# Performance work log

Hardware: AMD Instinct MI355X
Metric: run time of the kernel (lower is better)

Reference implementation:

```python
import jax, jax.numpy as jnp
import numpy as np

B, T, C = 2, 1024, 256
DH = 8          # deformable head num
HD = 64         # head_dim
HN = C // HD    # head_num = 4


def grid_sample_bilinear(img, grid):
    """torch.nn.functional.grid_sample (bilinear, align_corners=True) for a
    single-channel image. img: (B,H,W); grid: (B,Ho,Wo,2) with grid[...,0]=x
    (width coord), grid[...,1]=y (height coord), both in [-1,1]."""
    B_, H, W = img.shape
    gx = (grid[..., 0] + 1.0) * 0.5 * (W - 1)
    gy = (grid[..., 1] + 1.0) * 0.5 * (H - 1)
    x0 = jnp.floor(gx)
    y0 = jnp.floor(gy)
    wx = gx - x0
    wy = gy - y0
    flat_img = img.reshape(B_, -1)

    def gather(iy, ix):
        iy = jnp.clip(iy.astype(jnp.int32), 0, H - 1)
        ix = jnp.clip(ix.astype(jnp.int32), 0, W - 1)
        flat = (iy * W + ix).reshape(B_, -1)
        return jnp.take_along_axis(flat_img, flat, axis=1).reshape(iy.shape)

    out = (gather(y0, x0) * (1 - wy) * (1 - wx)
           + gather(y0, x0 + 1) * (1 - wy) * wx
           + gather(y0 + 1, x0) * wy * (1 - wx)
           + gather(y0 + 1, x0 + 1) * wy * wx)
    return out  # (B, Ho, Wo)


def setup_inputs() -> dict:
    key = jax.random.key(0)
    ks = jax.random.split(key, 8)
    s = 1.0 / np.sqrt(C)
    return {
        "x": jax.random.normal(ks[0], (B, T, C), jnp.float32),
        "W_off1": jax.random.normal(ks[1], (C, C), jnp.float32) * s,
        "b_off1": jnp.zeros((C,), jnp.float32),
        "W_off2": jax.random.normal(ks[2], (C, DH * C * 2), jnp.float32) * s,
        "b_off2": jnp.zeros((DH * C * 2,), jnp.float32),
        "Wq": jax.random.normal(ks[3], (C, C), jnp.float32) * s,
        "bq": jnp.zeros((C,), jnp.float32),
        "Wk": jax.random.normal(ks[4], (C, C), jnp.float32) * s,
        "bk": jnp.zeros((C,), jnp.float32),
        "Wv": jax.random.normal(ks[5], (C, C), jnp.float32) * s,
        "bv": jnp.zeros((C,), jnp.float32),
        "Wo": jax.random.normal(ks[6], (DH * C, C), jnp.float32) / np.sqrt(DH * C),
        "bo": jnp.zeros((C,), jnp.float32),
    }


def reference(x, W_off1, b_off1, W_off2, b_off2, Wq, bq, Wk, bk, Wv, bv, Wo, bo):
    B_, T_, C_ = x.shape
    # offset network: per-token MLP -> DH heads of (C,2) grid coords in [-1,1]
    h = jax.nn.gelu(x @ W_off1 + b_off1)
    off = jnp.tanh((h @ W_off2 + b_off2).reshape(B_, T_, DH, C_, 2))
    off = off.transpose(0, 2, 1, 3, 4).reshape(B_, DH * T_, C_, 2)
    # deformable token resampling: x tiled DH times along token axis acts as
    # a 1-channel image of size (DH*T, C); grid_sample(bilinear, align_corners)
    img = jnp.tile(x, (1, DH, 1))                       # B x (DH*T) x C
    xs = grid_sample_bilinear(img, off)                 # B x (DH*T) x C
    xs = xs.reshape(B_ * DH, T_, C_)
    # multi-head attention over resampled tokens
    q = (xs @ Wq + bq).reshape(B_ * DH, T_, HN, HD)
    k = (xs @ Wk + bk).reshape(B_ * DH, T_, HN, HD)
    v = (xs @ Wv + bv).reshape(B_ * DH, T_, HN, HD)
    scores = jnp.einsum('bnhd,bkhd->bhnk', q, k) / np.float32(np.sqrt(HD))
    A = jax.nn.softmax(scores, axis=-1)
    out = jnp.einsum('bhnk,bkhd->bnhd', A, v).reshape(B_ * DH, T_, HN * HD)
    # gather deformable heads back and project
    out = out.reshape(B_, DH, T_, HN * HD).transpose(0, 2, 1, 3).reshape(B_, T_, DH * HN * HD)
    return out @ Wo + bo
```

## Files before the change

### kernel.cpp

```cpp
#include <hip/hip_runtime.h>
#include <hip/hip_bf16.h>

typedef __attribute__((ext_vector_type(8))) _Float16 half8;
typedef __attribute__((ext_vector_type(4))) _Float16 half4;
typedef __attribute__((ext_vector_type(4))) float f32x4;
typedef __attribute__((ext_vector_type(16))) float f32x16;
typedef __attribute__((ext_vector_type(2))) unsigned uint2v;
typedef __attribute__((ext_vector_type(4))) unsigned uint4v;

#define MFMAH(a, b, c) __builtin_amdgcn_mfma_f32_16x16x32_f16((a), (b), (c), 0, 0, 0)
#define MFMA32(a, b, c) __builtin_amdgcn_mfma_f32_32x32x16_f16((a), (b), (c), 0, 0, 0)

__device__ __forceinline__ short f2h(float v) { _Float16 h = (_Float16)v; return __builtin_bit_cast(short, h); }
__device__ __forceinline__ f32x4 fzero() { f32x4 z = {0.f, 0.f, 0.f, 0.f}; return z; }
__device__ __forceinline__ float u2f(unsigned u) { return __builtin_bit_cast(float, u); }
__device__ __forceinline__ unsigned f2u(float f) { return __builtin_bit_cast(unsigned, f); }

__device__ __forceinline__ void gl16(const void* g, void* l) {
    __builtin_amdgcn_global_load_lds((const __attribute__((address_space(1))) unsigned*)g,
                                     (__attribute__((address_space(3))) unsigned*)l, 16, 0, 0);
}

__device__ __forceinline__ float fast_tanh(float z) {
    float E = __expf(2.f * z);
    return 1.f - 2.f / (E + 1.f);
}

__device__ __forceinline__ float gelu_tanh(float v) {
    float u = 0.7978845608028654f * (v + 0.044715f * v * v * v);
    return 0.5f * v * (1.f + fast_tanh(u));
}


__global__ __launch_bounds__(256) void prep_all_k(
    const float* __restrict__ x, const float* __restrict__ Woff2,
    const float* __restrict__ Wq, const float* __restrict__ Wk, const float* __restrict__ Wv,
    const float* __restrict__ Wo,
    short* __restrict__ B2T, short* __restrict__ Wtqkv, short* __restrict__ WtoT,
    half4* __restrict__ Q)
{
    __shared__ float t[64][65];
    const int tid = threadIdx.x;
    const int bid = blockIdx.x;
    if (bid < 256) {
        const int bk = bid >> 6, bn = bid & 63;
        const int k0 = bk * 64, n0 = bn * 64;
#pragma unroll
        for (int p = 0; p < 16; ++p) {
            int idx = p * 256 + tid, r = idx >> 6, c = idx & 63;
            t[r][c] = Woff2[(long)(k0 + r) * 4096 + n0 + c];
        }
        __syncthreads();
#pragma unroll
        for (int p = 0; p < 16; ++p) {
            int idx = p * 256 + tid, nr = idx >> 6, kc = idx & 63;
            float v = t[kc][nr];
            _Float16 w1 = (_Float16)v;
            _Float16 w2 = (_Float16)(v - (float)w1);
            long base = (long)(n0 + nr) * 768 + k0 + kc;
            B2T[base]       = __builtin_bit_cast(short, w1);
            B2T[base + 256] = __builtin_bit_cast(short, w1);
            B2T[base + 512] = __builtin_bit_cast(short, w2);
        }
    } else if (bid < 1024) {
        int i = (bid - 256) * 256 + tid;
        int n = i >> 8, k = i & 255;
        const float* s = (n < 256) ? Wq : (n < 512) ? Wk : Wv;
        Wtqkv[i] = f2h(s[k * 256 + (n & 255)]);
    } else if (bid < 3072) {
        int i = (bid - 1024) * 256 + tid;
        int n = i >> 11, k = i & 2047;
        WtoT[i] = f2h(Wo[k * 256 + n]);
    } else {
        int i = (bid - 3072) * 256 + tid;
        int b = i >> 18, r = (i >> 8) & 1023, c = i & 255;
        const float* xb = x + (b << 18);
        int r1 = (r + 1) & 1023, c1 = (c + 1) & 255;
        half4 qv;
        qv[0] = (_Float16)xb[(r << 8) + c];
        qv[1] = (_Float16)xb[(r << 8) + c1];
        qv[2] = (_Float16)xb[(r1 << 8) + c];
        qv[3] = (_Float16)xb[(r1 << 8) + c1];
        Q[i] = qv;
    }
}


__global__ __launch_bounds__(256) void gemm1_k(const float* __restrict__ x, const float* __restrict__ W,
                                               const float* __restrict__ bias, short* __restrict__ hs) {
    __shared__ float As[64][17];
    __shared__ float Bs[16][68];
    const int tid = threadIdx.x;
    const int bm = blockIdx.x >> 2, bn = blockIdx.x & 3;
    const int m0 = bm * 64, n0 = bn * 64;
    const int ty = tid >> 4, tx = tid & 15;
    float acc[4][4] = {};
    const int ar = tid >> 2, ak = (tid & 3) << 2;
    const int bk = tid >> 4, bc = (tid & 15) << 2;

    for (int k0 = 0; k0 < 256; k0 += 16) {
        __syncthreads();
        float4 av = *(const float4*)(x + (m0 + ar) * 256 + k0 + ak);
        As[ar][ak + 0] = av.x; As[ar][ak + 1] = av.y; As[ar][ak + 2] = av.z; As[ar][ak + 3] = av.w;
        *(float4*)&Bs[bk][bc] = *(const float4*)(W + (k0 + bk) * 256 + n0 + bc);
        __syncthreads();
#pragma unroll
        for (int kk = 0; kk < 16; ++kk) {
            float a_[4], b_[4];
#pragma unroll
            for (int i = 0; i < 4; ++i) a_[i] = As[ty * 4 + i][kk];
            *(float4*)b_ = *(const float4*)&Bs[kk][tx * 4];
#pragma unroll
            for (int i = 0; i < 4; ++i)
#pragma unroll
                for (int j = 0; j < 4; ++j) acc[i][j] += a_[i] * b_[j];
        }
    }
#pragma unroll
    for (int i = 0; i < 4; ++i) {
        int row = m0 + ty * 4 + i;
#pragma unroll
        for (int j = 0; j < 4; ++j) {
            int col = n0 + tx * 4 + j;
            float v = gelu_tanh(acc[i][j] + bias[col]);
            _Float16 h1 = (_Float16)v;
            _Float16 h2 = (_Float16)(v - (float)h1);
            hs[row * 768 + col]       = __builtin_bit_cast(short, h1);
            hs[row * 768 + 256 + col] = __builtin_bit_cast(short, h2);
            hs[row * 768 + 512 + col] = __builtin_bit_cast(short, h1);
        }
    }
}


__global__ __launch_bounds__(256, 3) void gemm_samp(
    const short* __restrict__ A, const short* __restrict__ BT,
    const float* __restrict__ b0, short* __restrict__ out0, const half4* __restrict__ Q)
{
    __shared__ short lds[16384];
    short* As0 = lds;
    short* As1 = lds + 4096;
    short* Bs0 = lds + 8192;
    short* Bs1 = lds + 12288;

    const int tid = threadIdx.x;
    const int lane = tid & 63, w = tid >> 6;
    const int rl = lane & 15, g = lane >> 4;
    const int wr = w >> 1, wc = w & 1;
    const int bid = blockIdx.x;
    const int g2 = bid & 7, s = bid >> 3;
    const int bm = (g2 >> 2) * 8 + (s >> 3);
    const int bn = (g2 & 3) * 8 + (s & 7);
    const int m0 = bm << 7, n0 = bn << 7;

    f32x4 acc[4][4];
#pragma unroll
    for (int m = 0; m < 4; ++m)
#pragma unroll
        for (int n = 0; n < 4; ++n) acc[m][n] = fzero();

    const short* ap = A + (long)(m0 + w * 32 + (lane >> 2)) * 768 + ((lane & 3) << 3);
    const short* bp = BT + (long)(n0 + w * 32 + (lane >> 2)) * 768 + ((lane & 3) << 3);
    const int woff = w * 1024;

#define STAGE(dA, dB, kk) do { \
        gl16(ap + (kk), (dA) + woff); \
        gl16(ap + (kk) + 16 * 768, (dA) + woff + 512); \
        gl16(bp + (kk), (dB) + woff); \
        gl16(bp + (kk) + 16 * 768, (dB) + woff + 512); } while (0)

    STAGE(As0, Bs0, 0);
    for (int t = 0; t < 24; ++t) {
        const short* cA = (t & 1) ? As1 : As0;
        const short* cB = (t & 1) ? Bs1 : Bs0;
        short* nA = (t & 1) ? As0 : As1;
        short* nB = (t & 1) ? Bs0 : Bs1;
        if (t + 1 < 24) {
            STAGE(nA, nB, (t + 1) << 5);
            asm volatile("s_waitcnt vmcnt(4)" ::: "memory");
        } else {
            asm volatile("s_waitcnt vmcnt(0)" ::: "memory");
        }
        __builtin_amdgcn_s_barrier();
        half8 af[4], bf[4];
#pragma unroll
        for (int m = 0; m < 4; ++m) af[m] = *(const half8*)&cA[(wr * 64 + m * 16 + rl) * 32 + g * 8];
#pragma unroll
        for (int n = 0; n < 4; ++n) bf[n] = *(const half8*)&cB[(wc * 64 + n * 16 + rl) * 32 + g * 8];
#pragma unroll
        for (int m = 0; m < 4; ++m)
#pragma unroll
            for (int n = 0; n < 4; ++n) acc[m][n] = MFMAH(af[m], bf[n], acc[m][n]);
        __builtin_amdgcn_s_barrier();
    }
#undef STAGE

    const int jlo = (rl & 1) ? 2 : 0;
#pragma unroll
    for (int m = 0; m < 4; ++m)
#pragma unroll
        for (int nt = 0; nt < 4; ++nt) {
            const int col = n0 + wc * 64 + nt * 16 + rl;
            float o4[4], po4[4];
            const float bb = b0[col];
#pragma unroll
            for (int j = 0; j < 4; ++j) o4[j] = fast_tanh(acc[m][nt][j] + bb);
#pragma unroll
            for (int j = 0; j < 4; ++j) po4[j] = __shfl_xor(o4[j], 1);
            const int cl = (wc * 64 + nt * 16 + rl) >> 1;
#pragma unroll
            for (int u = 0; u < 2; ++u) {
                const int j = jlo + u;
                float gx = (((rl & 1) ? po4[j] : o4[j]) + 1.f) * 127.5f;
                float gy = (((rl & 1) ? o4[j] : po4[j]) + 1.f) * 4095.5f;
                float x0f = floorf(gx), y0f = floorf(gy);
                float wx = gx - x0f, wy = gy - y0f;
                int ix0 = (int)x0f, iy0 = (int)y0f;
                const int rowl = wr * 64 + m * 16 + g * 4 + j;
                const int b = (m0 + rowl) >> 10;
                half4 qv = Q[((long)b << 18) + ((iy0 & 1023) << 8) + ix0];
                float r = (float)qv[0] * (1.f - wy) * (1.f - wx) + (float)qv[1] * (1.f - wy) * wx
                        + (float)qv[2] * wy * (1.f - wx) + (float)qv[3] * wy * wx;
                lds[rowl * 72 + cl] = f2h(r);
            }
        }
    __syncthreads();
    const int d = n0 >> 9, c0 = (n0 >> 1) & 255;
    const int b = m0 >> 10, t0 = m0 & 1023;
    short* xo = out0 + ((long)(b * 8 + d) * 1024 + t0) * 256 + c0;
#pragma unroll
    for (int p = 0; p < 4; ++p) {
        int idx = p * 256 + tid, rowl = idx >> 3, ch = idx & 7;
        *(half8*)(xo + rowl * 256 + ch * 8) = *(const half8*)&lds[rowl * 72 + ch * 8];
    }
}


template <int EPI>
__global__ __launch_bounds__(256, 3) void gemm128(
    const short* __restrict__ A, const short* __restrict__ BT,
    const float* __restrict__ b0, const float* __restrict__ b1, const float* __restrict__ b2,
    void* __restrict__ out0, void* __restrict__ out1, void* __restrict__ out2,
    int M, int N, int K, int lda, int ldb)
{
    __shared__ short lds[16384];
    short* As0 = lds;
    short* As1 = lds + 4096;
    short* Bs0 = lds + 8192;
    short* Bs1 = lds + 12288;

    const int tid = threadIdx.x;
    const int lane = tid & 63, w = tid >> 6;
    const int rl = lane & 15, g = lane >> 4;
    const int wr = w >> 1, wc = w & 1;
    const int bid = blockIdx.x;
    int bm, bn;
    if (EPI == 2) {
        int s = bid >> 3;
        bm = (bid & 7) * 16 + s / 6;
        bn = s - (s / 6) * 6;
    } else {
        const int nb = N >> 7;
        bm = bid / nb;
        bn = bid % nb;
    }
    const int m0 = bm << 7, n0 = bn << 7;

    if (EPI == 3) { A += blockIdx.y << 8; BT += blockIdx.y << 8; }

    f32x4 acc[4][4];
#pragma unroll
    for (int m = 0; m < 4; ++m)
#pragma unroll
        for (int n = 0; n < 4; ++n) acc[m][n] = fzero();

    const short* ap = A + (long)(m0 + w * 32 + (lane >> 2)) * lda + ((lane & 3) << 3);
    const short* bp = BT + (long)(n0 + w * 32 + (lane >> 2)) * ldb + ((lane & 3) << 3);
    const int woff = w * 1024;

#define STAGE(dA, dB, kk) do { \
        gl16(ap + (kk), (dA) + woff); \
        gl16(ap + (kk) + 16 * lda, (dA) + woff + 512); \
        gl16(bp + (kk), (dB) + woff); \
        gl16(bp + (kk) + 16 * ldb, (dB) + woff + 512); } while (0)

    const int nt_ = K >> 5;
    STAGE(As0, Bs0, 0);
    for (int t = 0; t < nt_; ++t) {
        const short* cA = (t & 1) ? As1 : As0;
        const short* cB = (t & 1) ? Bs1 : Bs0;
        short* nA = (t & 1) ? As0 : As1;
        short* nB = (t & 1) ? Bs0 : Bs1;
        if (t + 1 < nt_) {
            STAGE(nA, nB, (t + 1) << 5);
            asm volatile("s_waitcnt vmcnt(4)" ::: "memory");
        } else {
            asm volatile("s_waitcnt vmcnt(0)" ::: "memory");
        }
        __builtin_amdgcn_s_barrier();
        half8 af[4], bf[4];
#pragma unroll
        for (int m = 0; m < 4; ++m) af[m] = *(const half8*)&cA[(wr * 64 + m * 16 + rl) * 32 + g * 8];
#pragma unroll
        for (int n = 0; n < 4; ++n) bf[n] = *(const half8*)&cB[(wc * 64 + n * 16 + rl) * 32 + g * 8];
#pragma unroll
        for (int m = 0; m < 4; ++m)
#pragma unroll
            for (int n = 0; n < 4; ++n) acc[m][n] = MFMAH(af[m], bf[n], acc[m][n]);
        __builtin_amdgcn_s_barrier();
    }
#undef STAGE

    if (EPI == 2) {
#pragma unroll
        for (int m = 0; m < 4; ++m)
#pragma unroll
            for (int nt = 0; nt < 4; ++nt) {
                const int cl = wc * 64 + nt * 16 + rl;
                const int col = n0 + cl;
#pragma unroll
                for (int j = 0; j < 4; ++j) {
                    const int tl = wr * 64 + m * 16 + g * 4 + j;
                    float v;
                    int slot;
                    if (bn < 2) {
                        v = (acc[m][nt][j] + b0[col]) * 0.18033688011112042f;
                        slot = tl * 128 + cl;
                    } else if (bn < 4) {
                        v = acc[m][nt][j] + b1[(bn - 2) * 128 + cl];
                        int hl = cl >> 6, dd = cl & 63;
                        int c = dd >> 4, hi2 = (dd >> 3) & 1, e = dd & 7;
                        int kkl = tl >> 5, l31t = tl & 31;
                        slot = (hl * 4 + kkl) * 2048 + (c * 64 + hi2 * 32 + l31t) * 8 + e;
                    } else {
                        v = acc[m][nt][j] + b2[(bn - 4) * 128 + cl];
                        int hl = cl >> 6, d = cl & 63;
                        int kkl = tl >> 5, chi = (tl >> 4) & 1, hi2 = (tl >> 3) & 1, e = tl & 7;
                        int c = chi * 2 + (d >> 5);
                        slot = (hl * 4 + kkl) * 2048 + (c * 64 + hi2 * 32 + (d & 31)) * 8 + e;
                    }
                    lds[slot] = f2h(v);
                }
            }
        __syncthreads();
        const int bh = m0 >> 10;
        if (bn < 2) {
            short* qo = (short*)out0 + (long)m0 * 256 + n0;
#pragma unroll
            for (int p = 0; p < 8; ++p) {
                int idx = p * 256 + tid, rowl = idx >> 4, ch = idx & 15;
                *(half8*)(qo + rowl * 256 + ch * 8) = *(const half8*)&lds[rowl * 128 + ch * 8];
            }
        } else {
            short* dst = (bn < 4) ? (short*)out1 : (short*)out2;
            const int hb = (bn < 4) ? (bn - 2) * 2 : (bn - 4) * 2;
            const int kk0 = (m0 & 1023) >> 5;
#pragma unroll
            for (int p = 0; p < 8; ++p) {
                int idx = p * 256 + tid, til = idx >> 8, wit = idx & 255;
                int hl = til >> 2, kkl = til & 3;
                long base = (((long)(bh * 4 + hb + hl) * 32) + kk0 + kkl) * 2048;
                *(half8*)(dst + base + wit * 8) = *(const half8*)&lds[til * 2048 + wit * 8];
            }
        }
    } else {
        float* op = (float*)out0 + (long)blockIdx.y * M * N;
#pragma unroll
        for (int m = 0; m < 4; ++m)
#pragma unroll
            for (int nt = 0; nt < 4; ++nt) {
                const int col = n0 + wc * 64 + nt * 16 + rl;
#pragma unroll
                for (int j = 0; j < 4; ++j) {
                    const long grow = m0 + wr * 64 + m * 16 + g * 4 + j;
                    op[grow * N + col] = acc[m][nt][j];
                }
            }
    }
}

__global__ void reduce_out_k(const float* __restrict__ p, const float* __restrict__ bo,
                             float* __restrict__ out) {
    int i = blockIdx.x * 256 + threadIdx.x;
    float s = bo[i & 255];
#pragma unroll
    for (int ks = 0; ks < 8; ++ks) s += p[ks * 524288 + i];
    out[i] = s;
}


__global__ __launch_bounds__(256) void attn_k(const short* __restrict__ q, const short* __restrict__ kc,
                                              const short* __restrict__ vc, short* __restrict__ oc) {
    __shared__ short kv[12288];
    const int tid = threadIdx.x;
    const int lane = tid & 63, w = tid >> 6;
    const int l31 = lane & 31, hi = lane >> 5;
    const int bhh = blockIdx.x & 63;
    const int bh = bhh >> 2, h = bhh & 3;
    const int q0 = (blockIdx.x >> 6) * 128 + w * 32;

    const short* qb = q + (long)bh * 262144 + h * 64;
    const short* kt = kc + (long)bhh * 65536;
    const short* vt = vc + (long)bhh * 65536;

    half8 qf[4];
#pragma unroll
    for (int c = 0; c < 4; ++c)
        qf[c] = *(const half8*)(qb + (long)(q0 + l31) * 256 + c * 16 + hi * 8);

    float m_ = -1e30f, l_ = 0.f;
    f32x16 O0, O1;
#pragma unroll
    for (int r = 0; r < 16; ++r) { O0[r] = 0.f; O1[r] = 0.f; }

    const int sw = w * 512 + lane * 8;

#define KVSTAGE(kk, b) do { \
        gl16(kt + (kk) * 2048 + sw, &kv[(b) * 4096 + w * 512]); \
        gl16(vt + (kk) * 2048 + sw, &kv[(b) * 4096 + 2048 + w * 512]); } while (0)

    KVSTAGE(0, 0);
    KVSTAGE(1, 1);
    int bc = 0, bs = 2;
    for (int kk = 0; kk < 32; ++kk) {
        if (kk < 31) asm volatile("s_waitcnt vmcnt(2)" ::: "memory");
        else         asm volatile("s_waitcnt vmcnt(0)" ::: "memory");
        __builtin_amdgcn_s_barrier();
        if (kk + 2 < 32) {
            KVSTAGE(kk + 2, bs);
            bs = (bs == 2) ? 0 : bs + 1;
        }
        const int bb = bc * 4096;
        half8 KD[4], VD[4];
#pragma unroll
        for (int c = 0; c < 4; ++c) {
            KD[c] = *(const half8*)&kv[bb + c * 512 + lane * 8];
            VD[c] = *(const half8*)&kv[bb + 2048 + c * 512 + lane * 8];
        }
        f32x16 S;
#pragma unroll
        for (int r = 0; r < 16; ++r) S[r] = 0.f;
#pragma unroll
        for (int c = 0; c < 4; ++c) S = MFMA32(KD[c], qf[c], S);
        float t8[8];
#pragma unroll
        for (int r = 0; r < 8; ++r) t8[r] = fmaxf(S[2 * r], S[2 * r + 1]);
        float mx = fmaxf(fmaxf(fmaxf(t8[0], t8[1]), fmaxf(t8[2], t8[3])),
                         fmaxf(fmaxf(t8[4], t8[5]), fmaxf(t8[6], t8[7])));
        uint2v sp = __builtin_amdgcn_permlane32_swap(f2u(mx), f2u(mx), false, false);
        mx = fmaxf(u2f(sp[0]), u2f(sp[1]));
        if (__any(mx > m_ + 8.f)) {
            float mn = fmaxf(m_, mx);
            float sc = exp2f(m_ - mn);
            m_ = mn;
            l_ *= sc;
#pragma unroll
            for (int r = 0; r < 16; ++r) { O0[r] *= sc; O1[r] *= sc; }
        }
        float p[16];
#pragma unroll
        for (int r = 0; r < 16; ++r) p[r] = exp2f(S[r] - m_);
        float s8[8];
#pragma unroll
        for (int r = 0; r < 8; ++r) s8[r] = p[2 * r] + p[2 * r + 1];
        float rs = (((s8[0] + s8[1]) + (s8[2] + s8[3])) + ((s8[4] + s8[5]) + (s8[6] + s8[7])));
        uint2v sq = __builtin_amdgcn_permlane32_swap(f2u(rs), f2u(rs), false, false);
        rs = u2f(sq[0]) + u2f(sq[1]);
        l_ += rs;
        half8 PA[2];
#pragma unroll
        for (int c = 0; c < 2; ++c) {
            const int o = c * 8;
            unsigned a0 = f2u(__builtin_bit_cast(float, __builtin_amdgcn_cvt_pkrtz(p[o + 0], p[o + 1])));
            unsigned b0v = f2u(__builtin_bit_cast(float, __builtin_amdgcn_cvt_pkrtz(p[o + 4], p[o + 5])));
            unsigned a1 = f2u(__builtin_bit_cast(float, __builtin_amdgcn_cvt_pkrtz(p[o + 2], p[o + 3])));
            unsigned b1v = f2u(__builtin_bit_cast(float, __builtin_amdgcn_cvt_pkrtz(p[o + 6], p[o + 7])));
            uint2v r0 = __builtin_amdgcn_permlane32_swap(a0, b0v, false, false);
            uint2v r1 = __builtin_amdgcn_permlane32_swap(a1, b1v, false, false);
            uint4v wpk = {r0[0], r1[0], r0[1], r1[1]};
            PA[c] = __builtin_bit_cast(half8, wpk);
        }
        O0 = MFMA32(VD[0], PA[0], O0);
        O1 = MFMA32(VD[1], PA[0], O1);
        O0 = MFMA32(VD[2], PA[1], O0);
        O1 = MFMA32(VD[3], PA[1], O1);
        bc = (bc == 2) ? 0 : bc + 1;
    }
#undef KVSTAGE

    const float inv = 1.f / l_;
    const int b = bh >> 3, d = bh & 7;
    const int t = q0 + l31;
    short* ob = oc + ((long)(b * 1024 + t) * 8 + d) * 256 + h * 64;
#pragma unroll
    for (int rr = 0; rr < 8; ++rr) {
        int dvb = (rr & 1) * 2 + 8 * (rr >> 1) + 4 * hi;
        unsigned u0 = (unsigned short)f2h(O0[2 * rr] * inv) | ((unsigned)(unsigned short)f2h(O0[2 * rr + 1] * inv) << 16);
        unsigned u1 = (unsigned short)f2h(O1[2 * rr] * inv) | ((unsigned)(unsigned short)f2h(O1[2 * rr + 1] * inv) << 16);
        *(unsigned*)(ob + dvb) = u0;
        *(unsigned*)(ob + 32 + dvb) = u1;
    }
}


extern "C" void kernel_launch(void* const* d_in, const int* in_sizes, int n_in,
                              void* d_out, int out_size, void* d_ws, size_t ws_size,
                              hipStream_t stream) {
    const float* x     = (const float*)d_in[0];
    const float* Woff1 = (const float*)d_in[1];
    const float* boff1 = (const float*)d_in[2];
    const float* Woff2 = (const float*)d_in[3];
    const float* boff2 = (const float*)d_in[4];
    const float* Wq    = (const float*)d_in[5];
    const float* bq    = (const float*)d_in[6];
    const float* Wk    = (const float*)d_in[7];
    const float* bk    = (const float*)d_in[8];
    const float* Wv    = (const float*)d_in[9];
    const float* bv    = (const float*)d_in[10];
    const float* Wo    = (const float*)d_in[11];
    const float* bo    = (const float*)d_in[12];

    char* ws = (char*)d_ws;
    short* hsplit = (short*)(ws + 0);
    short* B2T    = (short*)(ws + 3145728);
    short* cat    = (short*)(ws + 0);
    short* Wtqkv  = (short*)(ws + 9437184);
    short* WtoT   = (short*)(ws + 9830400);
    short* xs     = (short*)(ws + 10878976);
    short* qbuf   = (short*)(ws + 19267584);
    short* kcoal  = (short*)(ws + 27656192);
    short* vcoal  = (short*)(ws + 36044800);
    half4* Qt     = (half4*)(ws + 44433408);
    float* parts  = (float*)(ws + 44433408);

    prep_all_k<<<5120, 256, 0, stream>>>(x, Woff2, Wq, Wk, Wv, Wo, B2T, Wtqkv, WtoT, Qt);

    gemm1_k<<<128, 256, 0, stream>>>(x, Woff1, boff1, hsplit);

    gemm_samp<<<512, 256, 0, stream>>>(hsplit, B2T, boff2, xs, Qt);

    gemm128<2><<<(16384 / 128) * (768 / 128), 256, 0, stream>>>(
        xs, Wtqkv, bq, bk, bv, qbuf, kcoal, vcoal, 16384, 768, 256, 256, 256);

    attn_k<<<512, 256, 0, stream>>>(qbuf, kcoal, vcoal, cat);

    gemm128<3><<<dim3((2048 / 128) * (256 / 128), 8), 256, 0, stream>>>(
        cat, WtoT, nullptr, nullptr, nullptr, parts, nullptr, nullptr, 2048, 256, 256, 2048, 2048);
    reduce_out_k<<<2048, 256, 0, stream>>>(parts, bo, (float*)d_out);
}
```

Before: 136.9 us.

## Split fused offset GEMM and grid-sample into separate GEMM and sampling kernels

The offset GEMM no longer applies tanh and bilinear sampling in its epilogue. It now writes raw fp32 offsets (2048x4096) to a workspace buffer through LDS staging, and a new sample_k kernel reads them, applies tanh, gathers from the quad table and writes the fp16 resampled tokens. The aim is to take the scattered gather latency out of the GEMM epilogue and run the sampling with a simpler, more parallel layout. The cost is an extra 32MB fp32 write and read, one more kernel launch, and workspace offsets that were reshuffled.

```diff
diff --git a/kernel.cpp b/kernel.cpp
--- a/kernel.cpp
+++ b/kernel.cpp
@@ -133,9 +133,9 @@
 }
 
 
-__global__ __launch_bounds__(256, 3) void gemm_samp(
+__global__ __launch_bounds__(256, 3) void gemm_off(
     const short* __restrict__ A, const short* __restrict__ BT,
-    const float* __restrict__ b0, short* __restrict__ out0, const half4* __restrict__ Q)
+    const float* __restrict__ b0, float* __restrict__ oz)
 {
     __shared__ short lds[16384];
     short* As0 = lds;
@@ -195,44 +195,60 @@
     }
 #undef STAGE
 
-    const int jlo = (rl & 1) ? 2 : 0;
-#pragma unroll
-    for (int m = 0; m < 4; ++m)
-#pragma unroll
-        for (int nt = 0; nt < 4; ++nt) {
-            const int col = n0 + wc * 64 + nt * 16 + rl;
-            float o4[4], po4[4];
-            const float bb = b0[col];
-#pragma unroll
-            for (int j = 0; j < 4; ++j) o4[j] = fast_tanh(acc[m][nt][j] + bb);
-#pragma unroll
-            for (int j = 0; j < 4; ++j) po4[j] = __shfl_xor(o4[j], 1);
-            const int cl = (wc * 64 + nt * 16 + rl) >> 1;
-#pragma unroll
-            for (int u = 0; u < 2; ++u) {
-                const int j = jlo + u;
-                float gx = (((rl & 1) ? po4[j] : o4[j]) + 1.f) * 127.5f;
-                float gy = (((rl & 1) ? o4[j] : po4[j]) + 1.f) * 4095.5f;
-                float x0f = floorf(gx), y0f = floorf(gy);
-                float wx = gx - x0f, wy = gy - y0f;
-                int ix0 = (int)x0f, iy0 = (int)y0f;
-                const int rowl = wr * 64 + m * 16 + g * 4 + j;
-                const int b = (m0 + rowl) >> 10;
-                half4 qv = Q[((long)b << 18) + ((iy0 & 1023) << 8) + ix0];
-                float r = (float)qv[0] * (1.f - wy) * (1.f - wx) + (float)qv[1] * (1.f - wy) * wx
-                        + (float)qv[2] * wy * (1.f - wx) + (float)qv[3] * wy * wx;
-                lds[rowl * 72 + cl] = f2h(r);
-            }
-        }
-    __syncthreads();
-    const int d = n0 >> 9, c0 = (n0 >> 1) & 255;
-    const int b = m0 >> 10, t0 = m0 & 1023;
-    short* xo = out0 + ((long)(b * 8 + d) * 1024 + t0) * 256 + c0;
-#pragma unroll
-    for (int p = 0; p < 4; ++p) {
-        int idx = p * 256 + tid, rowl = idx >> 3, ch = idx & 7;
-        *(half8*)(xo + rowl * 256 + ch * 8) = *(const half8*)&lds[rowl * 72 + ch * 8];
-    }
+    float* ldsf = (float*)lds;
+#pragma unroll
+    for (int pass = 0; pass < 2; ++pass) {
+        __syncthreads();
+        if (wr == pass) {
+#pragma unroll
+            for (int m = 0; m < 4; ++m)
+#pragma unroll
+                for (int nt = 0; nt < 4; ++nt) {
+                    const int cl = wc * 64 + nt * 16 + rl;
+                    const float bb = b0[n0 + cl];
+#pragma unroll
+                    for (int j = 0; j < 4; ++j)
+                        ldsf[(m * 16 + g * 4 + j) * 128 + cl] = acc[m][nt][j] + bb;
+                }
+        }
+        __syncthreads();
+        float* oo = oz + (long)(m0 + pass * 64) * 4096 + n0;
+#pragma unroll
+        for (int p = 0; p < 8; ++p) {
+            int idx = p * 256 + tid, rowl = idx >> 5, ch = idx & 31;
+            *(float4*)(oo + rowl * 4096 + ch * 4) = *(const float4*)&ldsf[rowl * 128 + ch * 4];
+        }
+    }
+}
+
+
+__global__ __launch_bounds__(256) void sample_k(const float* __restrict__ oz,
+                                                const half4* __restrict__ Q,
+                                                short* __restrict__ xs) {
+    const int tid = threadIdx.x, bid = blockIdx.x;
+    const int xcd = bid & 7, batch = xcd >> 2;
+    const int t = (xcd & 3) * 256 + (bid >> 3);
+    const int d = tid >> 5, c0 = (tid & 31) * 8;
+    const float* orow = oz + (long)(batch * 1024 + t) * 4096 + d * 512 + c0 * 2;
+    float o[16];
+    *(float4*)&o[0]  = *(const float4*)(orow + 0);
+    *(float4*)&o[4]  = *(const float4*)(orow + 4);
+    *(float4*)&o[8]  = *(const float4*)(orow + 8);
+    *(float4*)&o[12] = *(const float4*)(orow + 12);
+    const half4* Qb = Q + ((long)batch << 18);
+    short res[8];
+#pragma unroll
+    for (int i = 0; i < 8; ++i) {
+        float gx = (fast_tanh(o[2 * i]) + 1.f) * 127.5f;
+        float gy = (fast_tanh(o[2 * i + 1]) + 1.f) * 4095.5f;
+        float x0f = floorf(gx), y0f = floorf(gy);
+        float wx = gx - x0f, wy = gy - y0f;
+        int ix0 = (int)x0f, iy0 = (int)y0f;
+        half4 qv = Qb[((iy0 & 1023) << 8) + ix0];
+        res[i] = f2h((float)qv[0] * (1.f - wy) * (1.f - wx) + (float)qv[1] * (1.f - wy) * wx
+                   + (float)qv[2] * wy * (1.f - wx) + (float)qv[3] * wy * wx);
+    }
+    *(half8*)(xs + ((long)(batch * 8 + d) * 1024 + t) * 256 + c0) = *(half8*)res;
 }
 
 
@@ -526,18 +542,21 @@
     short* cat    = (short*)(ws + 0);
     short* Wtqkv  = (short*)(ws + 9437184);
     short* WtoT   = (short*)(ws + 9830400);
-    short* xs     = (short*)(ws + 10878976);
-    short* qbuf   = (short*)(ws + 19267584);
-    short* kcoal  = (short*)(ws + 27656192);
-    short* vcoal  = (short*)(ws + 36044800);
-    half4* Qt     = (half4*)(ws + 44433408);
-    float* parts  = (float*)(ws + 44433408);
+    half4* Qt     = (half4*)(ws + 10878976);
+    short* xs     = (short*)(ws + 15073280);
+    float* oz     = (float*)(ws + 23461888);
+    short* qbuf   = (short*)(ws + 23461888);
+    short* kcoal  = (short*)(ws + 31850496);
+    short* vcoal  = (short*)(ws + 40239104);
+    float* parts  = (float*)(ws + 48627712);
 
     prep_all_k<<<5120, 256, 0, stream>>>(x, Woff2, Wq, Wk, Wv, Wo, B2T, Wtqkv, WtoT, Qt);
 
     gemm1_k<<<128, 256, 0, stream>>>(x, Woff1, boff1, hsplit);
 
-    gemm_samp<<<512, 256, 0, stream>>>(hsplit, B2T, boff2, xs, Qt);
+    gemm_off<<<512, 256, 0, stream>>>(hsplit, B2T, boff2, oz);
+
+    sample_k<<<2048, 256, 0, stream>>>(oz, Qt, xs);
 
     gemm128<2><<<(16384 / 128) * (768 / 128), 256, 0, stream>>>(
         xs, Wtqkv, bq, bk, bv, qbuf, kcoal, vcoal, 16384, 768, 256, 256, 256);
```

Measured after the change: 140.8 us. +2.9%, slower.
